# Performance work log

Measured on AMD Instinct MI355X. Metric: run time of the kernel, lower is better.

## Reference

```python
import jax, jax.numpy as jnp
import numpy as np

T = 20            # tagset size
START = 17
END = 18
COST_VALUE = 1.0
CHEM_COLS = jnp.array([0, 1, 2, 3])  # S/B/I/E-CHEMICAL destination tags
L, B = 512, 128


def setup_inputs() -> dict:
    key = jax.random.key(0)
    k1, k2, k3 = jax.random.split(key, 3)
    trellis = jax.random.normal(k1, (L, B, T, T), dtype=jnp.float32)
    gold = jax.random.randint(k2, (L, B, 1), 0, T * T, dtype=jnp.int64)
    lengths = jax.random.randint(k3, (B,), 1, L + 1)
    mask = (jnp.arange(L)[:, None] < lengths[None, :])  # (L, B) bool, monotone
    corpus_mask = jnp.ones((1, 1, 1, 1), dtype=bool)     # unused (change_gold=False)
    return {"trellis": trellis, "gold": gold, "mask": mask, "corpus_mask": corpus_mask}


def _crf_loss(trellis, gold, mask):
    seq_len, bat_size = trellis.shape[:2]

    # gold energy: gather from UN-augmented trellis, masked sum
    flat = trellis.reshape(seq_len, bat_size, T * T)
    energy = jnp.take_along_axis(flat, gold, axis=2)[..., 0]     # (L, B)
    gold_energy = jnp.sum(jnp.where(mask, energy, 0.0))

    # augmented cost: +cost_value on CHEMICAL destination columns for t >= 1
    cost_vec = jnp.zeros((T,), trellis.dtype).at[CHEM_COLS].set(COST_VALUE)
    step_on = (jnp.arange(seq_len) > 0).astype(trellis.dtype)
    aug = trellis + step_on[:, None, None, None] * cost_vec      # (L,B,T,T)

    # forward algorithm (log-sum-exp scan over the 'from' dim)
    partition0 = aug[0, :, START, :]                              # (B, T)

    def step(part, inp):
        cur, m = inp                                              # (B,T,T), (B,)
        cur_vals = cur + part[:, :, None]                         # broadcast over 'to'
        cur_part = jax.nn.logsumexp(cur_vals, axis=1)             # (B, T)
        part = jnp.where(m[:, None], cur_part, part)
        return part, None

    part, _ = jax.lax.scan(step, partition0, (aug[1:], mask[1:]))
    partition = part[:, END].sum()
    return (partition - gold_energy) / bat_size


def reference(trellis, gold, mask, corpus_mask):
    return _crf_loss(trellis, gold, mask)
```

## Files before the change

kernel.cpp:

```cpp
#include <hip/hip_runtime.h>

#define TS 20
#define TT 400
#define NB 128
#define NL 512
#define HALF 256
#define S_START 17
#define S_END 18
#define CSTRIDE 21
#define CBWORDS 536
#define LSTRIDE (NB * TT)
#define LOG2E 1.4426950408889634f
#define LN2 0.6931471805599453f

#define WS_GOLD 0
#define WS_FS 16
#define WS_FL 160
#define WS_BS 2720
#define WS_BL 2848

__device__ __forceinline__ float rfl_f(float x) {
    return __int_as_float(__builtin_amdgcn_readfirstlane(__float_as_int(x)));
}

__global__ __launch_bounds__(64, 1) void crf_chain(const float* __restrict__ tr,
                                                   const unsigned char* __restrict__ mask8,
                                                   const int* __restrict__ mask32,
                                                   const int* __restrict__ gold32,
                                                   float* __restrict__ wsf) {
    const int lane = threadIdx.x;

    const bool isu8 = (mask8[1] == 1);
    int o = 0;
    #pragma unroll
    for (int k = 1; k < 32; k += 2) o |= gold32[k];
    const bool is64 = (o == 0);

    if (blockIdx.x >= 256) {
        const int gb = blockIdx.x - 256;
        float v = 0.0f;
        #pragma unroll
        for (int t = 0; t < 4; ++t) {
            int idx = gb * 256 + t * 64 + lane;
            int m = isu8 ? (int)mask8[idx] : mask32[idx];
            if (m) {
                int g = is64 ? gold32[2 * idx] : gold32[idx];
                g = max(0, min(g, TT - 1));
                v += tr[(size_t)idx * TT + g];
            }
        }
        #pragma unroll
        for (int off = 32; off; off >>= 1) v += __shfl_down(v, off);
        if (lane == 0) atomicAdd(wsf + WS_GOLD, v);
        return;
    }

    __shared__ float cbuf[2][CBWORDS];

    const int b = blockIdx.x >> 1;
    const int dir = blockIdx.x & 1;
    const float* trb = tr + (size_t)b * TT;

    int cnt = 0;
    #pragma unroll
    for (int t = 0; t < 8; ++t) {
        size_t l = lane + 64 * t;
        cnt += isu8 ? (mask8[l * NB + b] ? 1 : 0) : (mask32[l * NB + b] ? 1 : 0);
    }
    #pragma unroll
    for (int off = 1; off < 64; off <<= 1) cnt += __shfl_xor(cnt, off);
    const int len = max(1, min(cnt, NL));

    const int jc = (lane < TS) ? lane : (TS - 1);
    const int jcs = jc * CSTRIDE;
    float s, q;
    if (dir == 0) {
        float t0 = trb[S_START * TS + jc];
        float ref = rfl_f(t0);
        s = ref; q = __expf(t0 - ref);
    } else {
        s = 0.0f; q = (jc == S_END) ? 1.0f : 0.0f;
    }
    float qs[TS];
    #pragma unroll
    for (int i = 0; i < TS; ++i)
        qs[i] = __int_as_float(__builtin_amdgcn_readlane(__float_as_int(q), i));

    const int fB = min(64 + lane, 99);
    int dA[4], dB[4];
    float cA[4], cB[4];
    #pragma unroll
    for (int c = 0; c < 4; ++c) {
        int nA = 4 * lane + c;
        int iA = nA / TS, jA = nA - iA * TS;
        dA[c] = (dir == 0) ? (jA * CSTRIDE + iA) : (iA * CSTRIDE + jA);
        cA[c] = (jA < 4) ? LOG2E : 0.0f;
        if (lane < 36) {
            int nB = 256 + 4 * lane + c;
            int iB = nB / TS, jB = nB - iB * TS;
            dB[c] = (dir == 0) ? (jB * CSTRIDE + iB) : (iB * CSTRIDE + jB);
            cB[c] = (jB < 4) ? LOG2E : 0.0f;
        } else {
            dB[c] = 420 + (lane - 36) * 4 + c;
            cB[c] = 0.0f;
        }
    }

    #define STAGE_TILE(dst, A, B)                                              \
        do {                                                                   \
            (dst)[dA[0]] = __builtin_amdgcn_exp2f(fmaf((A).x, LOG2E, cA[0]));  \
            (dst)[dA[1]] = __builtin_amdgcn_exp2f(fmaf((A).y, LOG2E, cA[1]));  \
            (dst)[dA[2]] = __builtin_amdgcn_exp2f(fmaf((A).z, LOG2E, cA[2]));  \
            (dst)[dA[3]] = __builtin_amdgcn_exp2f(fmaf((A).w, LOG2E, cA[3]));  \
            (dst)[dB[0]] = __builtin_amdgcn_exp2f(fmaf((B).x, LOG2E, cB[0])); \
            (dst)[dB[1]] = __builtin_amdgcn_exp2f(fmaf((B).y, LOG2E, cB[1])); \
            (dst)[dB[2]] = __builtin_amdgcn_exp2f(fmaf((B).z, LOG2E, cB[2])); \
            (dst)[dB[3]] = __builtin_amdgcn_exp2f(fmaf((B).w, LOG2E, cB[3])); \
        } while (0)

    const int S = (dir == 0) ? (min(len, HALF) - 1) : max(len - HALF, 0);

    if (S > 0) {
        #define LROW(t) ((dir == 0) ? (1 + (t)) : (len - 1 - (t)))
        float4 A0, B0, A1, B1, A2, B2, A3, B3, A4, B4, A5, B5;
        #define LOAD_TILE(t, A, B)                                             \
            do {                                                               \
                int row_ = LROW(min((t), S - 1));                              \
                const float4* tp_ = (const float4*)(trb + (size_t)row_ * LSTRIDE); \
                A = tp_[lane];                                                 \
                B = tp_[fB];                                                   \
            } while (0)
        LOAD_TILE(0, A0, B0);
        LOAD_TILE(1, A1, B1);
        LOAD_TILE(2, A2, B2);
        LOAD_TILE(3, A3, B3);
        LOAD_TILE(4, A4, B4);
        LOAD_TILE(5, A5, B5);
        STAGE_TILE(&cbuf[0][0], A0, B0);

        #define STEP(U, LA, LB, SA, SB, RB, WB)                                \
        {                                                                      \
            LOAD_TILE((U) + 6, LA, LB);                 \
            float w[TS];                                                       \
            _Pragma("unroll")                                                  \
            for (int i = 0; i < TS; ++i) w[i] = cbuf[RB][jcs + i];             \
            STAGE_TILE(&cbuf[WB][0], SA, SB);              \
            float a0 = qs[0] * w[0];                                           \
            float a1 = qs[1] * w[1];                                           \
            float a2 = qs[2] * w[2];                                           \
            float a3 = qs[3] * w[3];                                           \
            a0 = fmaf(qs[4],  w[4],  a0);  a1 = fmaf(qs[5],  w[5],  a1);       \
            a2 = fmaf(qs[6],  w[6],  a2);  a3 = fmaf(qs[7],  w[7],  a3);       \
            a0 = fmaf(qs[8],  w[8],  a0);  a1 = fmaf(qs[9],  w[9],  a1);       \
            a2 = fmaf(qs[10], w[10], a2);  a3 = fmaf(qs[11], w[11], a3);       \
            a0 = fmaf(qs[12], w[12], a0);  a1 = fmaf(qs[13], w[13], a1);       \
            a2 = fmaf(qs[14], w[14], a2);  a3 = fmaf(qs[15], w[15], a3);       \
            a0 = fmaf(qs[16], w[16], a0);  a1 = fmaf(qs[17], w[17], a1);       \
            a2 = fmaf(qs[18], w[18], a2);  a3 = fmaf(qs[19], w[19], a3);       \
            float acc = (a0 + a1) + (a2 + a3);                                 \
            int ebits = __builtin_amdgcn_readfirstlane(__float_as_int(acc));   \
            int e = ((ebits >> 23) & 255) - 127;                               \
            bool live = (U) < S;                                               \
            s = live ? fmaf((float)e, LN2, s) : s;                             \
            q = live ? (acc * __int_as_float((127 - e) << 23)) : q;            \
            _Pragma("unroll")                                                  \
            for (int i = 0; i < TS; ++i)                                       \
                qs[i] = __int_as_float(                                        \
                    __builtin_amdgcn_readlane(__float_as_int(q), i));          \
        }

        const int nsteps = ((S + 5) / 6) * 6;
        for (int u = 0; u < nsteps; u += 6) {
            STEP(u + 0, A0, B0, A1, B1, 0, 1);
            STEP(u + 1, A1, B1, A2, B2, 1, 0);
            STEP(u + 2, A2, B2, A3, B3, 0, 1);
            STEP(u + 3, A3, B3, A4, B4, 1, 0);
            STEP(u + 4, A4, B4, A5, B5, 0, 1);
            STEP(u + 5, A5, B5, A0, B0, 1, 0);
        }
        #undef STEP
        #undef LOAD_TILE
        #undef LROW
    }

    float lq = __logf(q);

    float* ss = wsf + ((dir == 0) ? WS_FS : WS_BS);
    float* ll = wsf + ((dir == 0) ? WS_FL : WS_BL);
    if (lane == 0) ss[b] = s;
    if (lane < TS) ll[b * TS + lane] = lq;
}

__global__ __launch_bounds__(128) void crf_merge(const float* __restrict__ wsf,
                                                 float* __restrict__ out) {
    const int b = threadIdx.x;
    const float* fl = wsf + WS_FL + b * TS;
    const float* bl = wsf + WS_BL + b * TS;
    float v[TS];
    float m = -3e38f;
    #pragma unroll
    for (int i = 0; i < TS; ++i) { v[i] = fl[i] + bl[i]; m = fmaxf(m, v[i]); }
    float sum = 0.0f;
    #pragma unroll
    for (int i = 0; i < TS; ++i) sum += __expf(v[i] - m);
    float part = wsf[WS_FS + b] + wsf[WS_BS + b] + m + __logf(sum);
    #pragma unroll
    for (int off = 32; off; off >>= 1) part += __shfl_down(part, off);
    __shared__ float ps[2];
    if ((threadIdx.x & 63) == 0) ps[threadIdx.x >> 6] = part;
    __syncthreads();
    if (threadIdx.x == 0) out[0] = (ps[0] + ps[1] - wsf[WS_GOLD]) / 128.0f;
}

extern "C" void kernel_launch(void* const* d_in, const int* in_sizes, int n_in,
                              void* d_out, int out_size, void* d_ws, size_t ws_size,
                              hipStream_t stream) {
    const float* tr = (const float*)d_in[0];
    const int* gold32 = (const int*)d_in[1];
    const unsigned char* mask8 = (const unsigned char*)d_in[2];
    const int* mask32 = (const int*)d_in[2];
    float* wsf = (float*)d_ws;
    float* out = (float*)d_out;

    hipMemsetAsync(d_ws, 0, 64, stream);
    crf_chain<<<512, 64, 0, stream>>>(tr, mask8, mask32, gold32, wsf);
    crf_merge<<<1, 128, 0, stream>>>(wsf, out);
}
```

Measured before the change: 207.1 us.

## Hand-schedule global loads with inline asm, prefetch weights, and renormalize every sixth step

Replaces compiler-generated tile loads with inline-asm global_load_dwordx4 plus explicit s_waitcnt vmcnt(10), so six tiles stay in flight without the compiler inserting conservative waits. The LDS stride is widened to 36 so each lane's 20 weights can be read as five aligned float4 vector loads. Next step's weights are read right after staging, one step ahead of use, to hide LDS latency behind the FMA chain. Renormalization with readfirstlane now runs once every six steps instead of every step, shortening the serial dependency chain at some risk of float overflow or underflow between renorms.

```diff
diff --git a/kernel.cpp b/kernel.cpp
--- a/kernel.cpp
+++ b/kernel.cpp
@@ -7,8 +7,8 @@
 #define HALF 256
 #define S_START 17
 #define S_END 18
-#define CSTRIDE 21
-#define CBWORDS 536
+#define CSTRIDE 36
+#define CBWORDS 832
 #define LSTRIDE (NB * TT)
 #define LOG2E 1.4426950408889634f
 #define LN2 0.6931471805599453f
@@ -18,6 +18,9 @@
 #define WS_FL 160
 #define WS_BS 2720
 #define WS_BL 2848
+
+typedef float f32x4 __attribute__((ext_vector_type(4)));
+struct W5 { f32x4 r0, r1, r2, r3, r4; };
 
 __device__ __forceinline__ float rfl_f(float x) {
     return __int_as_float(__builtin_amdgcn_readfirstlane(__float_as_int(x)));
@@ -101,82 +104,99 @@
             dB[c] = (dir == 0) ? (jB * CSTRIDE + iB) : (iB * CSTRIDE + jB);
             cB[c] = (jB < 4) ? LOG2E : 0.0f;
         } else {
-            dB[c] = 420 + (lane - 36) * 4 + c;
+            dB[c] = 720 + (lane - 36) * 4 + c;
             cB[c] = 0.0f;
         }
     }
 
-    #define STAGE_TILE(dst, A, B)                                              \
-        do {                                                                   \
-            (dst)[dA[0]] = __builtin_amdgcn_exp2f(fmaf((A).x, LOG2E, cA[0]));  \
-            (dst)[dA[1]] = __builtin_amdgcn_exp2f(fmaf((A).y, LOG2E, cA[1]));  \
-            (dst)[dA[2]] = __builtin_amdgcn_exp2f(fmaf((A).z, LOG2E, cA[2]));  \
-            (dst)[dA[3]] = __builtin_amdgcn_exp2f(fmaf((A).w, LOG2E, cA[3]));  \
-            (dst)[dB[0]] = __builtin_amdgcn_exp2f(fmaf((B).x, LOG2E, cB[0])); \
-            (dst)[dB[1]] = __builtin_amdgcn_exp2f(fmaf((B).y, LOG2E, cB[1])); \
-            (dst)[dB[2]] = __builtin_amdgcn_exp2f(fmaf((B).z, LOG2E, cB[2])); \
-            (dst)[dB[3]] = __builtin_amdgcn_exp2f(fmaf((B).w, LOG2E, cB[3])); \
+    #define STAGE_TILE(dst, A, B)                                                \
+        do {                                                                     \
+            (dst)[dA[0]] = __builtin_amdgcn_exp2f(fmaf((A)[0], LOG2E, cA[0]));   \
+            (dst)[dA[1]] = __builtin_amdgcn_exp2f(fmaf((A)[1], LOG2E, cA[1]));   \
+            (dst)[dA[2]] = __builtin_amdgcn_exp2f(fmaf((A)[2], LOG2E, cA[2]));   \
+            (dst)[dA[3]] = __builtin_amdgcn_exp2f(fmaf((A)[3], LOG2E, cA[3]));   \
+            (dst)[dB[0]] = __builtin_amdgcn_exp2f(fmaf((B)[0], LOG2E, cB[0]));   \
+            (dst)[dB[1]] = __builtin_amdgcn_exp2f(fmaf((B)[1], LOG2E, cB[1]));   \
+            (dst)[dB[2]] = __builtin_amdgcn_exp2f(fmaf((B)[2], LOG2E, cB[2]));   \
+            (dst)[dB[3]] = __builtin_amdgcn_exp2f(fmaf((B)[3], LOG2E, cB[3]));   \
         } while (0)
 
     const int S = (dir == 0) ? (min(len, HALF) - 1) : max(len - HALF, 0);
 
     if (S > 0) {
         #define LROW(t) ((dir == 0) ? (1 + (t)) : (len - 1 - (t)))
-        float4 A0, B0, A1, B1, A2, B2, A3, B3, A4, B4, A5, B5;
-        #define LOAD_TILE(t, A, B)                                             \
-            do {                                                               \
-                int row_ = LROW(min((t), S - 1));                              \
-                const float4* tp_ = (const float4*)(trb + (size_t)row_ * LSTRIDE); \
-                A = tp_[lane];                                                 \
-                B = tp_[fB];                                                   \
+        f32x4 A0, B0, A1, B1, A2, B2, A3, B3, A4, B4, A5, B5;
+        W5 wa, wb;
+
+        #define LOAD_TILE(t, A, B)                                               \
+            do {                                                                 \
+                int row_ = LROW(min((t), S - 1));                                \
+                const float* rp_ = trb + (size_t)row_ * LSTRIDE;                 \
+                unsigned long long aA_ = (unsigned long long)(rp_ + 4 * lane);   \
+                unsigned long long aB_ = (unsigned long long)(rp_ + 4 * fB);     \
+                asm volatile("global_load_dwordx4 %0, %1, off"                   \
+                             : "=v"(A) : "v"(aA_));                              \
+                asm volatile("global_load_dwordx4 %0, %1, off"                   \
+                             : "=v"(B) : "v"(aB_));                              \
             } while (0)
+
         LOAD_TILE(0, A0, B0);
         LOAD_TILE(1, A1, B1);
         LOAD_TILE(2, A2, B2);
         LOAD_TILE(3, A3, B3);
         LOAD_TILE(4, A4, B4);
         LOAD_TILE(5, A5, B5);
+        asm volatile("s_waitcnt vmcnt(10)" : "+v"(A0), "+v"(B0));
         STAGE_TILE(&cbuf[0][0], A0, B0);
-
-        #define STEP(U, LA, LB, SA, SB, RB, WB)                                \
-        {                                                                      \
-            LOAD_TILE((U) + 6, LA, LB);                 \
-            float w[TS];                                                       \
-            _Pragma("unroll")                                                  \
-            for (int i = 0; i < TS; ++i) w[i] = cbuf[RB][jcs + i];             \
-            STAGE_TILE(&cbuf[WB][0], SA, SB);              \
-            float a0 = qs[0] * w[0];                                           \
-            float a1 = qs[1] * w[1];                                           \
-            float a2 = qs[2] * w[2];                                           \
-            float a3 = qs[3] * w[3];                                           \
-            a0 = fmaf(qs[4],  w[4],  a0);  a1 = fmaf(qs[5],  w[5],  a1);       \
-            a2 = fmaf(qs[6],  w[6],  a2);  a3 = fmaf(qs[7],  w[7],  a3);       \
-            a0 = fmaf(qs[8],  w[8],  a0);  a1 = fmaf(qs[9],  w[9],  a1);       \
-            a2 = fmaf(qs[10], w[10], a2);  a3 = fmaf(qs[11], w[11], a3);       \
-            a0 = fmaf(qs[12], w[12], a0);  a1 = fmaf(qs[13], w[13], a1);       \
-            a2 = fmaf(qs[14], w[14], a2);  a3 = fmaf(qs[15], w[15], a3);       \
-            a0 = fmaf(qs[16], w[16], a0);  a1 = fmaf(qs[17], w[17], a1);       \
-            a2 = fmaf(qs[18], w[18], a2);  a3 = fmaf(qs[19], w[19], a3);       \
-            float acc = (a0 + a1) + (a2 + a3);                                 \
-            int ebits = __builtin_amdgcn_readfirstlane(__float_as_int(acc));   \
-            int e = ((ebits >> 23) & 255) - 127;                               \
-            bool live = (U) < S;                                               \
-            s = live ? fmaf((float)e, LN2, s) : s;                             \
-            q = live ? (acc * __int_as_float((127 - e) << 23)) : q;            \
-            _Pragma("unroll")                                                  \
-            for (int i = 0; i < TS; ++i)                                       \
-                qs[i] = __int_as_float(                                        \
-                    __builtin_amdgcn_readlane(__float_as_int(q), i));          \
+        {
+            const f32x4* rp_ = (const f32x4*)&cbuf[0][jcs];
+            wa.r0 = rp_[0]; wa.r1 = rp_[1]; wa.r2 = rp_[2]; wa.r3 = rp_[3]; wa.r4 = rp_[4];
+        }
+
+        #define STEP(U, LA, LB, SA, SB, WB, WC, WN, RENORM)                      \
+        {                                                                        \
+            LOAD_TILE((U) + 6, LA, LB);                                          \
+            asm volatile("s_waitcnt vmcnt(10)" : "+v"(SA), "+v"(SB));            \
+            STAGE_TILE(&cbuf[WB][0], SA, SB);                                    \
+            {                                                                    \
+                const f32x4* rp_ = (const f32x4*)&cbuf[WB][jcs];                 \
+                WN.r0 = rp_[0]; WN.r1 = rp_[1]; WN.r2 = rp_[2];                  \
+                WN.r3 = rp_[3]; WN.r4 = rp_[4];                                  \
+            }                                                                    \
+            float a0 = qs[0] * WC.r0[0];                                         \
+            float a1 = qs[1] * WC.r0[1];                                         \
+            float a2 = qs[2] * WC.r0[2];                                         \
+            float a3 = qs[3] * WC.r0[3];                                         \
+            a0 = fmaf(qs[4],  WC.r1[0], a0);  a1 = fmaf(qs[5],  WC.r1[1], a1);   \
+            a2 = fmaf(qs[6],  WC.r1[2], a2);  a3 = fmaf(qs[7],  WC.r1[3], a3);   \
+            a0 = fmaf(qs[8],  WC.r2[0], a0);  a1 = fmaf(qs[9],  WC.r2[1], a1);   \
+            a2 = fmaf(qs[10], WC.r2[2], a2);  a3 = fmaf(qs[11], WC.r2[3], a3);   \
+            a0 = fmaf(qs[12], WC.r3[0], a0);  a1 = fmaf(qs[13], WC.r3[1], a1);   \
+            a2 = fmaf(qs[14], WC.r3[2], a2);  a3 = fmaf(qs[15], WC.r3[3], a3);   \
+            a0 = fmaf(qs[16], WC.r4[0], a0);  a1 = fmaf(qs[17], WC.r4[1], a1);   \
+            a2 = fmaf(qs[18], WC.r4[2], a2);  a3 = fmaf(qs[19], WC.r4[3], a3);   \
+            float acc = (a0 + a1) + (a2 + a3);                                   \
+            q = ((U) < S) ? acc : q;                  \
+            if (RENORM) {                     \
+                int eb_ = __builtin_amdgcn_readfirstlane(__float_as_int(q));     \
+                int e_ = ((eb_ >> 23) & 255) - 127;                              \
+                s = fmaf((float)e_, LN2, s);                                     \
+                q = q * __int_as_float((127 - e_) << 23);    \
+            }                                                                    \
+            _Pragma("unroll")                                                    \
+            for (int i = 0; i < TS; ++i)                                         \
+                qs[i] = __int_as_float(                                          \
+                    __builtin_amdgcn_readlane(__float_as_int(q), i));            \
         }
 
         const int nsteps = ((S + 5) / 6) * 6;
         for (int u = 0; u < nsteps; u += 6) {
-            STEP(u + 0, A0, B0, A1, B1, 0, 1);
-            STEP(u + 1, A1, B1, A2, B2, 1, 0);
-            STEP(u + 2, A2, B2, A3, B3, 0, 1);
-            STEP(u + 3, A3, B3, A4, B4, 1, 0);
-            STEP(u + 4, A4, B4, A5, B5, 0, 1);
-            STEP(u + 5, A5, B5, A0, B0, 1, 0);
+            STEP(u + 0, A0, B0, A1, B1, 1, wa, wb, 0);
+            STEP(u + 1, A1, B1, A2, B2, 0, wb, wa, 0);
+            STEP(u + 2, A2, B2, A3, B3, 1, wa, wb, 0);
+            STEP(u + 3, A3, B3, A4, B4, 0, wb, wa, 0);
+            STEP(u + 4, A4, B4, A5, B5, 1, wa, wb, 0);
+            STEP(u + 5, A5, B5, A0, B0, 0, wb, wa, 1);
         }
         #undef STEP
         #undef LOAD_TILE
```

After: 195.8 us. -5.5%, faster.
